# Optimization experiments

Measured on AMD Instinct MI355X. Metric: run time of the kernel, lower is better.

## Reference

```python
import jax, jax.numpy as jnp
import numpy as np

B, CIN, COUT, H, W = 64, 64, 64, 32, 32
K, STRIDE, PAD = 3, 1, 1
HOUT = (H + 2 * PAD - K) // STRIDE + 1
WOUT = (W + 2 * PAD - K) // STRIDE + 1


def setup_inputs() -> dict:
    key = jax.random.key(0)
    k1, k2, k3 = jax.random.split(key, 3)
    x = jax.random.normal(k1, (B, CIN, H, W), dtype=jnp.float32)
    # weight: per-location filters (leading singleton batch dim of the torch
    # param is dropped; it only served broadcasting)
    weight = jax.random.normal(k2, (CIN, COUT, HOUT, WOUT, K, K), dtype=jnp.float32)
    bias = jax.random.normal(k3, (COUT, HOUT, WOUT), dtype=jnp.float32)
    return {"x": x, "weight": weight, "bias": bias}


def _extract_patches(x, k, stride, pad, hout, wout):
    # x: [B, C, H, W] -> patches [B, C, k*k, hout, wout]
    xp = jnp.pad(x, ((0, 0), (0, 0), (pad, pad), (pad, pad)))
    slabs = [
        xp[:, :, i : i + (hout - 1) * stride + 1 : stride,
               j : j + (wout - 1) * stride + 1 : stride]
        for i in range(k) for j in range(k)
    ]
    return jnp.stack(slabs, axis=2)


def reference(x, weight, bias):
    cin, cout, hout, wout, k, _ = weight.shape
    patches = _extract_patches(x, k, STRIDE, PAD, hout, wout)  # [B, Cin, k*k, Ho, Wo]
    w = weight.reshape(cin, cout, hout, wout, k * k)
    # fused per-location dot product: avoids the [B,Cin,Cout,Ho,Wo,k,k] intermediate
    y = jnp.einsum('bikhw,iohwk->bohw', patches, w) + bias[None]
    return y
```

## Files before the change

### kernel.cpp

```cpp
#include <hip/hip_runtime.h>
#include <hip/hip_bf16.h>


#define B_    64
#define HW_   32
#define HP_   34
#define NLOC  1024
#define W_OST 9216u
#define W_IST 589824u
#define XT_BYTES  ((size_t)64*HP_*HP_*64*2)
#define AF_BYTES  ((size_t)NLOC*18*4*64*16)
#define WS_NEED   (XT_BYTES + AF_BYTES)

typedef __attribute__((ext_vector_type(8))) short short8;
typedef __attribute__((ext_vector_type(8))) unsigned short ushort8;
typedef __attribute__((ext_vector_type(4))) float floatx4;

static __device__ __forceinline__ unsigned short f2bf(float f) {
  __hip_bfloat16 h = __float2bfloat16(f);
  return __builtin_bit_cast(unsigned short, h);
}

__global__ __launch_bounds__(256) void xpose_pad(const float* __restrict__ x,
                                                 unsigned short* __restrict__ xt) {
  int bid = blockIdx.x;
  int i = bid / HP_, hh = bid % HP_;
  __shared__ float tile[B_ * 33];
  int t = threadIdx.x;
  bool interior = (hh >= 1 && hh <= HW_);
  if (interior) {
    int h = hh - 1, w = t & 31, bs = t >> 5;
    #pragma unroll
    for (int r = 0; r < 8; ++r) {
      int b = r * 8 + bs;
      tile[b * 33 + w] = x[(((size_t)b * 64 + i) * HW_ + h) * HW_ + w];
    }
  }
  __syncthreads();
  int b = t & 63, wsb = t >> 6;
  size_t base = (size_t)(i * HP_ + hh) * HP_ * B_;
  #pragma unroll
  for (int s = 0; s < 9; ++s) {
    int ww = s * 4 + wsb;
    if (ww < HP_) {
      float v = 0.f;
      if (interior && ww >= 1 && ww <= HW_) v = tile[b * 33 + (ww - 1)];
      xt[base + (size_t)ww * B_ + b] = f2bf(v);
    }
  }
}

__global__ __launch_bounds__(256) void im2col_frag(
    const unsigned short* __restrict__ xt,
    unsigned short* __restrict__ af) {
  __shared__ unsigned short scr[4][512];
  const int bid  = blockIdx.x;
  const int loc  = ((bid & 7) << 7) | (bid >> 3);
  const int hblk = loc >> 5, wblk = loc & 31;
  const int tid  = threadIdx.x;
  const int lane = tid & 63;
  const int wv   = tid >> 6;

  #pragma unroll 1
  for (int c = 0; c < 18; ++c) {
    int i, kh, kw;
    if (c < 16) {
      i = (c << 2) + wv;
      int kk = lane >> 3;
      kh = kk / 3; kw = kk - kh * 3;
    } else {
      i = (c - 16) * 32 + wv * 8 + (lane >> 3);
      kh = 2; kw = 2;
    }
    const ushort8* src = (const ushort8*)(xt +
        (((unsigned)i * HP_ + (unsigned)(hblk + kh)) * HP_ + (unsigned)(wblk + kw)) * 64u
        + ((unsigned)(lane & 7) << 3));
    ushort8 v = *src;
    *(ushort8*)&scr[wv][lane << 3] = v;
    __asm__ volatile("s_waitcnt lgkmcnt(0)" ::: "memory");
    ushort8 p;
    #pragma unroll
    for (int jr = 0; jr < 8; ++jr) p[jr] = scr[wv][jr * 64 + lane];
    __asm__ volatile("s_waitcnt lgkmcnt(0)" ::: "memory");
    size_t slot = ((size_t)(loc * 18 + c) * 4 + (size_t)(lane >> 4)) * 64
                + (size_t)((lane & 15) + (wv << 4));
    *(ushort8*)(af + (slot << 3)) = p;
  }
}

__global__ __launch_bounds__(512, 2) void lc2d_fused(
    const unsigned short* __restrict__ af,
    const float* __restrict__ wsrc,
    const float* __restrict__ bias,
    float* __restrict__ out) {
  __shared__ unsigned short Bf[2][4 * 4 * 64 * 8];
  __shared__ unsigned short Bs[4 * 2 * 4 * 64 * 8];

  const int bid  = blockIdx.x;
  const int loc0 = bid << 2;
  const int tid  = threadIdx.x;
  const int lane = tid & 63;
  const int wv8  = tid >> 6;
  const int ll   = wv8 >> 1;
  const int nh   = wv8 & 1;
  const int loc  = loc0 + ll;
  const int col  = lane & 15;
  const int quad = lane >> 4;
  const int o_0  = nh * 32 + col;

  floatx4 acc[4][2];
  {
    float b0 = bias[(unsigned)o_0 * 1024u + (unsigned)loc];
    float b1 = bias[(unsigned)(o_0 + 16) * 1024u + (unsigned)loc];
    #pragma unroll
    for (int mt = 0; mt < 4; ++mt) {
      acc[mt][0] = (floatx4){b0, b0, b0, b0};
      acc[mt][1] = (floatx4){b1, b1, b1, b1};
    }
  }

  floatx4 wreg[5];
  const bool lastok = (tid < 256);
  const size_t wrow = (size_t)loc0 * 9;

  auto issueW = [&](int c) {
    const int i0 = c << 2;
    #pragma unroll
    for (int r = 0; r < 5; ++r) {
      if (r < 4 || lastok) {
        int idx = r * 512 + tid;
        int g = idx / 9, p = idx - g * 9;
        int i = i0 + (g >> 6), o = g & 63;
        wreg[r] = *(const floatx4*)(wsrc + (size_t)i * W_IST + (size_t)o * W_OST
                                    + wrow + (size_t)(p * 4));
      }
    }
  };
  auto scatterW = [&](int c, int buf) {
    const int i0 = c << 2;
    #pragma unroll
    for (int r = 0; r < 5; ++r) {
      if (r < 4 || lastok) {
        int idx = r * 512 + tid;
        int g = idx / 9, p = idx - g * 9;
        int iq = g >> 6, o = g & 63;
        int ot = o >> 4, oc = o & 15;
        int flane = iq * 16 + oc;
        #pragma unroll
        for (int e = 0; e < 4; ++e) {
          int fi = p * 4 + e;
          int lle = fi / 9, kk = fi - lle * 9;
          unsigned short v = f2bf(wreg[r][e]);
          if (kk < 8) {
            Bf[buf][((lle * 4 + ot) * 64 + flane) * 8 + kk] = v;
          } else {
            int i = i0 + iq;
            int sc = i >> 5, k2 = i & 31;
            Bs[((lle * 8 + sc * 4 + ot) * 64 + (k2 >> 3) * 16 + oc) * 8 + (k2 & 7)] = v;
          }
        }
      }
    }
  };

  const size_t abase = (size_t)loc * (18 * 4 * 64 * 8) + ((size_t)lane << 3);
  auto ldA = [&](int c, int tl) {
    return *(const ushort8*)(af + abase + ((size_t)(c * 4 + tl) << 9));
  };

  ushort8 pa0 = ldA(0, 0), pa1 = ldA(0, 1), pa2 = ldA(0, 2), pa3 = ldA(0, 3);

  issueW(0);
  scatterW(0, 0);
  __syncthreads();

  int buf = 0;
  #pragma unroll 1
  for (int c = 0; c < 16; ++c) {
    if (c < 15) issueW(c + 1);
    ushort8 a0 = pa0, a1 = pa1, a2 = pa2, a3 = pa3;
    pa0 = ldA(c + 1, 0); pa1 = ldA(c + 1, 1);
    pa2 = ldA(c + 1, 2); pa3 = ldA(c + 1, 3);
    ushort8 b0 = *(const ushort8*)&Bf[buf][((ll * 4 + nh * 2 + 0) * 64 + lane) * 8];
    ushort8 b1 = *(const ushort8*)&Bf[buf][((ll * 4 + nh * 2 + 1) * 64 + lane) * 8];
    acc[0][0] = __builtin_amdgcn_mfma_f32_16x16x32_bf16(
        __builtin_bit_cast(short8, a0), __builtin_bit_cast(short8, b0), acc[0][0], 0, 0, 0);
    acc[1][0] = __builtin_amdgcn_mfma_f32_16x16x32_bf16(
        __builtin_bit_cast(short8, a1), __builtin_bit_cast(short8, b0), acc[1][0], 0, 0, 0);
    acc[2][0] = __builtin_amdgcn_mfma_f32_16x16x32_bf16(
        __builtin_bit_cast(short8, a2), __builtin_bit_cast(short8, b0), acc[2][0], 0, 0, 0);
    acc[3][0] = __builtin_amdgcn_mfma_f32_16x16x32_bf16(
        __builtin_bit_cast(short8, a3), __builtin_bit_cast(short8, b0), acc[3][0], 0, 0, 0);
    acc[0][1] = __builtin_amdgcn_mfma_f32_16x16x32_bf16(
        __builtin_bit_cast(short8, a0), __builtin_bit_cast(short8, b1), acc[0][1], 0, 0, 0);
    acc[1][1] = __builtin_amdgcn_mfma_f32_16x16x32_bf16(
        __builtin_bit_cast(short8, a1), __builtin_bit_cast(short8, b1), acc[1][1], 0, 0, 0);
    acc[2][1] = __builtin_amdgcn_mfma_f32_16x16x32_bf16(
        __builtin_bit_cast(short8, a2), __builtin_bit_cast(short8, b1), acc[2][1], 0, 0, 0);
    acc[3][1] = __builtin_amdgcn_mfma_f32_16x16x32_bf16(
        __builtin_bit_cast(short8, a3), __builtin_bit_cast(short8, b1), acc[3][1], 0, 0, 0);
    if (c < 15) scatterW(c + 1, buf ^ 1);
    __syncthreads();
    buf ^= 1;
  }

  #pragma unroll
  for (int sc = 0; sc < 2; ++sc) {
    ushort8 a0 = pa0, a1 = pa1, a2 = pa2, a3 = pa3;
    if (sc == 0) { pa0 = ldA(17, 0); pa1 = ldA(17, 1); pa2 = ldA(17, 2); pa3 = ldA(17, 3); }
    ushort8 b0 = *(const ushort8*)&Bs[((ll * 8 + sc * 4 + nh * 2 + 0) * 64 + lane) * 8];
    ushort8 b1 = *(const ushort8*)&Bs[((ll * 8 + sc * 4 + nh * 2 + 1) * 64 + lane) * 8];
    acc[0][0] = __builtin_amdgcn_mfma_f32_16x16x32_bf16(
        __builtin_bit_cast(short8, a0), __builtin_bit_cast(short8, b0), acc[0][0], 0, 0, 0);
    acc[1][0] = __builtin_amdgcn_mfma_f32_16x16x32_bf16(
        __builtin_bit_cast(short8, a1), __builtin_bit_cast(short8, b0), acc[1][0], 0, 0, 0);
    acc[2][0] = __builtin_amdgcn_mfma_f32_16x16x32_bf16(
        __builtin_bit_cast(short8, a2), __builtin_bit_cast(short8, b0), acc[2][0], 0, 0, 0);
    acc[3][0] = __builtin_amdgcn_mfma_f32_16x16x32_bf16(
        __builtin_bit_cast(short8, a3), __builtin_bit_cast(short8, b0), acc[3][0], 0, 0, 0);
    acc[0][1] = __builtin_amdgcn_mfma_f32_16x16x32_bf16(
        __builtin_bit_cast(short8, a0), __builtin_bit_cast(short8, b1), acc[0][1], 0, 0, 0);
    acc[1][1] = __builtin_amdgcn_mfma_f32_16x16x32_bf16(
        __builtin_bit_cast(short8, a1), __builtin_bit_cast(short8, b1), acc[1][1], 0, 0, 0);
    acc[2][1] = __builtin_amdgcn_mfma_f32_16x16x32_bf16(
        __builtin_bit_cast(short8, a2), __builtin_bit_cast(short8, b1), acc[2][1], 0, 0, 0);
    acc[3][1] = __builtin_amdgcn_mfma_f32_16x16x32_bf16(
        __builtin_bit_cast(short8, a3), __builtin_bit_cast(short8, b1), acc[3][1], 0, 0, 0);
  }

  #pragma unroll
  for (int mt = 0; mt < 4; ++mt) {
    int b = mt * 16 + quad * 4;
    #pragma unroll
    for (int r = 0; r < 4; ++r) {
      out[((unsigned)(b + r) * 64u + (unsigned)o_0) * 1024u + (unsigned)loc] = acc[mt][0][r];
      out[((unsigned)(b + r) * 64u + (unsigned)(o_0 + 16)) * 1024u + (unsigned)loc] = acc[mt][1][r];
    }
  }
}

__global__ __launch_bounds__(256, 4) void lc2d_fallback(
    const float* __restrict__ x, const float* __restrict__ weight,
    const float* __restrict__ bias, float* __restrict__ out) {
  int t0 = blockIdx.x;
  int loc = ((t0 & 7) << 7) | (t0 >> 3);
  int h = loc >> 5, w = loc & 31;
  int tid = threadIdx.x;
  int b = tid & 63;
  int o0 = (tid >> 6) * 16;
  __shared__ float As[72 * 64];
  float acc[16];
  #pragma unroll
  for (int j = 0; j < 16; ++j) acc[j] = bias[(size_t)(o0 + j) * NLOC + loc];
  for (int ic = 0; ic < 8; ++ic) {
    __syncthreads();
    #pragma unroll
    for (int s = 0; s < 18; ++s) {
      int f = s * 256 + tid;
      int k = f >> 6, lb = f & 63;
      int kk = k >> 3, isub = k & 7;
      int i = ic * 8 + isub;
      int kh = kk / 3, kw = kk - kh * 3;
      int hh = h + kh - 1, ww = w + kw - 1;
      float v = (hh >= 0 && hh < HW_ && ww >= 0 && ww < HW_)
                  ? x[(((size_t)lb * 64 + i) * HW_ + hh) * HW_ + ww] : 0.f;
      As[k * 64 + lb] = v;
    }
    __syncthreads();
    #pragma unroll 1
    for (int isub = 0; isub < 8; ++isub) {
      const float* wp = weight + (size_t)(ic * 8 + isub) * W_IST
                               + (size_t)o0 * W_OST + loc * 9;
      #pragma unroll
      for (int kk = 0; kk < 9; ++kk) {
        float a = As[(kk * 8 + isub) * 64 + b];
        #pragma unroll
        for (int j = 0; j < 16; ++j)
          acc[j] = fmaf(a, wp[(size_t)j * W_OST + kk], acc[j]);
      }
    }
  }
  size_t ob = ((size_t)b * 64 + o0) * NLOC + loc;
  #pragma unroll
  for (int j = 0; j < 16; ++j) out[ob + (size_t)j * NLOC] = acc[j];
}

extern "C" void kernel_launch(void* const* d_in, const int* in_sizes, int n_in,
                              void* d_out, int out_size, void* d_ws, size_t ws_size,
                              hipStream_t stream) {
  const float* x  = (const float*)d_in[0];
  const float* wt = (const float*)d_in[1];
  const float* bs = (const float*)d_in[2];
  float* out = (float*)d_out;

  if (ws_size >= WS_NEED) {
    unsigned short* xtb = (unsigned short*)d_ws;
    unsigned short* af  = (unsigned short*)((char*)d_ws + XT_BYTES);
    xpose_pad<<<64 * HP_, 256, 0, stream>>>(x, xtb);
    im2col_frag<<<NLOC, 256, 0, stream>>>(xtb, af);
    lc2d_fused<<<NLOC / 4, 512, 0, stream>>>(af, wt, bs, out);
  } else {
    lc2d_fallback<<<NLOC, 256, 0, stream>>>(x, wt, bs, out);
  }
}
```

Before: 286.9 us.

## Fuse im2col fragment build into the locally-connected MFMA kernel

```diff
diff --git a/kernel.cpp b/kernel.cpp
--- a/kernel.cpp
+++ b/kernel.cpp
@@ -9,8 +9,7 @@
 #define W_OST 9216u
 #define W_IST 589824u
 #define XT_BYTES  ((size_t)64*HP_*HP_*64*2)
-#define AF_BYTES  ((size_t)NLOC*18*4*64*16)
-#define WS_NEED   (XT_BYTES + AF_BYTES)
+#define WS_NEED   (XT_BYTES)
 
 typedef __attribute__((ext_vector_type(8))) short short8;
 typedef __attribute__((ext_vector_type(8))) unsigned short ushort8;
@@ -50,51 +49,15 @@
   }
 }
 
-__global__ __launch_bounds__(256) void im2col_frag(
+__global__ __launch_bounds__(512, 2) void lc2d_fused(
     const unsigned short* __restrict__ xt,
-    unsigned short* __restrict__ af) {
-  __shared__ unsigned short scr[4][512];
-  const int bid  = blockIdx.x;
-  const int loc  = ((bid & 7) << 7) | (bid >> 3);
-  const int hblk = loc >> 5, wblk = loc & 31;
-  const int tid  = threadIdx.x;
-  const int lane = tid & 63;
-  const int wv   = tid >> 6;
-
-  #pragma unroll 1
-  for (int c = 0; c < 18; ++c) {
-    int i, kh, kw;
-    if (c < 16) {
-      i = (c << 2) + wv;
-      int kk = lane >> 3;
-      kh = kk / 3; kw = kk - kh * 3;
-    } else {
-      i = (c - 16) * 32 + wv * 8 + (lane >> 3);
-      kh = 2; kw = 2;
-    }
-    const ushort8* src = (const ushort8*)(xt +
-        (((unsigned)i * HP_ + (unsigned)(hblk + kh)) * HP_ + (unsigned)(wblk + kw)) * 64u
-        + ((unsigned)(lane & 7) << 3));
-    ushort8 v = *src;
-    *(ushort8*)&scr[wv][lane << 3] = v;
-    __asm__ volatile("s_waitcnt lgkmcnt(0)" ::: "memory");
-    ushort8 p;
-    #pragma unroll
-    for (int jr = 0; jr < 8; ++jr) p[jr] = scr[wv][jr * 64 + lane];
-    __asm__ volatile("s_waitcnt lgkmcnt(0)" ::: "memory");
-    size_t slot = ((size_t)(loc * 18 + c) * 4 + (size_t)(lane >> 4)) * 64
-                + (size_t)((lane & 15) + (wv << 4));
-    *(ushort8*)(af + (slot << 3)) = p;
-  }
-}
-
-__global__ __launch_bounds__(512, 2) void lc2d_fused(
-    const unsigned short* __restrict__ af,
     const float* __restrict__ wsrc,
     const float* __restrict__ bias,
     float* __restrict__ out) {
-  __shared__ unsigned short Bf[2][4 * 4 * 64 * 8];
-  __shared__ unsigned short Bs[4 * 2 * 4 * 64 * 8];
+  __shared__ __align__(16) unsigned short Af[2][4 * 4 * 64 * 8];
+  __shared__ __align__(16) unsigned short Bf[2][4 * 4 * 64 * 8];
+  __shared__ __align__(16) unsigned short Bs[4 * 2 * 4 * 64 * 8];
+  __shared__ __align__(16) unsigned short scr[8][512];
 
   const int bid  = blockIdx.x;
   const int loc0 = bid << 2;
@@ -104,6 +67,7 @@
   const int ll   = wv8 >> 1;
   const int nh   = wv8 & 1;
   const int loc  = loc0 + ll;
+  const int hblk = loc >> 5, wblk = loc & 31;
   const int col  = lane & 15;
   const int quad = lane >> 4;
   const int o_0  = nh * 32 + col;
@@ -119,11 +83,11 @@
     }
   }
 
-  floatx4 wreg[5];
+  floatx4 wa[5], wb[5];
   const bool lastok = (tid < 256);
   const size_t wrow = (size_t)loc0 * 9;
 
-  auto issueW = [&](int c) {
+  auto issueW = [&](int c, floatx4 (&wreg)[5]) {
     const int i0 = c << 2;
     #pragma unroll
     for (int r = 0; r < 5; ++r) {
@@ -136,7 +100,7 @@
       }
     }
   };
-  auto scatterW = [&](int c, int buf) {
+  auto scatterW = [&](int c, floatx4 (&wreg)[5], unsigned short* bfp) {
     const int i0 = c << 2;
     #pragma unroll
     for (int r = 0; r < 5; ++r) {
@@ -152,7 +116,7 @@
           int lle = fi / 9, kk = fi - lle * 9;
           unsigned short v = f2bf(wreg[r][e]);
           if (kk < 8) {
-            Bf[buf][((lle * 4 + ot) * 64 + flane) * 8 + kk] = v;
+            bfp[((lle * 4 + ot) * 64 + flane) * 8 + kk] = v;
           } else {
             int i = i0 + iq;
             int sc = i >> 5, k2 = i & 31;
@@ -163,26 +127,40 @@
     }
   };
 
-  const size_t abase = (size_t)loc * (18 * 4 * 64 * 8) + ((size_t)lane << 3);
-  auto ldA = [&](int c, int tl) {
-    return *(const ushort8*)(af + abase + ((size_t)(c * 4 + tl) << 9));
-  };
-
-  ushort8 pa0 = ldA(0, 0), pa1 = ldA(0, 1), pa2 = ldA(0, 2), pa3 = ldA(0, 3);
-
-  issueW(0);
-  scatterW(0, 0);
-  __syncthreads();
-
-  int buf = 0;
-  #pragma unroll 1
-  for (int c = 0; c < 16; ++c) {
-    if (c < 15) issueW(c + 1);
-    ushort8 a0 = pa0, a1 = pa1, a2 = pa2, a3 = pa3;
-    pa0 = ldA(c + 1, 0); pa1 = ldA(c + 1, 1);
-    pa2 = ldA(c + 1, 2); pa3 = ldA(c + 1, 3);
-    ushort8 b0 = *(const ushort8*)&Bf[buf][((ll * 4 + nh * 2 + 0) * 64 + lane) * 8];
-    ushort8 b1 = *(const ushort8*)&Bf[buf][((ll * 4 + nh * 2 + 1) * 64 + lane) * 8];
+  auto xtLoad = [&](int t, int s) -> ushort8 {
+    int q = (nh << 1) + s;
+    int i, kh, kw;
+    if (t < 16) {
+      i = (t << 2) + q;
+      int kk = lane >> 3;
+      kh = kk / 3; kw = kk - kh * 3;
+    } else {
+      i = ((t - 16) << 5) + (q << 3) + (lane >> 3);
+      kh = 2; kw = 2;
+    }
+    return *(const ushort8*)(xt +
+        (((unsigned)i * HP_ + (unsigned)(hblk + kh)) * HP_ + (unsigned)(wblk + kw)) * 64u
+        + ((unsigned)(lane & 7) << 3));
+  };
+  auto xposeStore = [&](ushort8 v, int s, unsigned short* afp) {
+    const int q = (nh << 1) + s;
+    *(ushort8*)&scr[wv8][lane << 3] = v;
+    __asm__ volatile("s_waitcnt lgkmcnt(0)" ::: "memory");
+    ushort8 p;
+    #pragma unroll
+    for (int jr = 0; jr < 8; ++jr) p[jr] = scr[wv8][jr * 64 + lane];
+    __asm__ volatile("s_waitcnt lgkmcnt(0)" ::: "memory");
+    *(ushort8*)(afp + (size_t)((((ll << 2) + (lane >> 4)) << 6)
+                               + (q << 4) + (lane & 15)) * 8) = p;
+  };
+
+  auto doMFMA = [&](const unsigned short* afp, const unsigned short* bbase, int boff) {
+    ushort8 a0 = *(const ushort8*)(afp + (size_t)(((ll << 2) + 0) * 64 + lane) * 8);
+    ushort8 a1 = *(const ushort8*)(afp + (size_t)(((ll << 2) + 1) * 64 + lane) * 8);
+    ushort8 a2 = *(const ushort8*)(afp + (size_t)(((ll << 2) + 2) * 64 + lane) * 8);
+    ushort8 a3 = *(const ushort8*)(afp + (size_t)(((ll << 2) + 3) * 64 + lane) * 8);
+    ushort8 b0 = *(const ushort8*)(bbase + (size_t)((boff + 0) * 64 + lane) * 8);
+    ushort8 b1 = *(const ushort8*)(bbase + (size_t)((boff + 1) * 64 + lane) * 8);
     acc[0][0] = __builtin_amdgcn_mfma_f32_16x16x32_bf16(
         __builtin_bit_cast(short8, a0), __builtin_bit_cast(short8, b0), acc[0][0], 0, 0, 0);
     acc[1][0] = __builtin_amdgcn_mfma_f32_16x16x32_bf16(
@@ -199,33 +177,46 @@
         __builtin_bit_cast(short8, a2), __builtin_bit_cast(short8, b1), acc[2][1], 0, 0, 0);
     acc[3][1] = __builtin_amdgcn_mfma_f32_16x16x32_bf16(
         __builtin_bit_cast(short8, a3), __builtin_bit_cast(short8, b1), acc[3][1], 0, 0, 0);
-    if (c < 15) scatterW(c + 1, buf ^ 1);
+  };
+
+  issueW(0, wa);
+  {
+    ushort8 pv0 = xtLoad(0, 0);
+    ushort8 pv1 = xtLoad(0, 1);
+    xposeStore(pv0, 0, &Af[0][0]);
+    xposeStore(pv1, 1, &Af[0][0]);
+  }
+  scatterW(0, wa, &Bf[0][0]);
+  issueW(1, wb);
+  __syncthreads();
+
+#define STEP(C, WI, WS) do {                                                  \
+    const int c_ = (C);                                                       \
+    ushort8 xv0 = xtLoad(c_ + 1, 0);                                          \
+    ushort8 xv1 = xtLoad(c_ + 1, 1);                                          \
+    if (c_ + 2 <= 15) issueW(c_ + 2, WI);                                     \
+    doMFMA(&Af[c_ & 1][0], &Bf[c_ & 1][0], (ll << 2) + (nh << 1));            \
+    xposeStore(xv0, 0, &Af[(c_ & 1) ^ 1][0]);                                 \
+    xposeStore(xv1, 1, &Af[(c_ & 1) ^ 1][0]);                                 \
+    if (c_ + 1 <= 15) scatterW(c_ + 1, WS, &Bf[(c_ & 1) ^ 1][0]);             \
+    __syncthreads();                                                          \
+  } while (0)
+
+  #pragma unroll 1
+  for (int cc = 0; cc < 16; cc += 2) {
+    STEP(cc,     wa, wb);
+    STEP(cc + 1, wb, wa);
+  }
+#undef STEP
+
+  {
+    ushort8 xv0 = xtLoad(17, 0);
+    ushort8 xv1 = xtLoad(17, 1);
+    doMFMA(&Af[0][0], &Bs[0], (ll << 3) + 0 + (nh << 1));
+    xposeStore(xv0, 0, &Af[1][0]);
+    xposeStore(xv1, 1, &Af[1][0]);
     __syncthreads();
-    buf ^= 1;
-  }
-
-  #pragma unroll
-  for (int sc = 0; sc < 2; ++sc) {
-    ushort8 a0 = pa0, a1 = pa1, a2 = pa2, a3 = pa3;
-    if (sc == 0) { pa0 = ldA(17, 0); pa1 = ldA(17, 1); pa2 = ldA(17, 2); pa3 = ldA(17, 3); }
-    ushort8 b0 = *(const ushort8*)&Bs[((ll * 8 + sc * 4 + nh * 2 + 0) * 64 + lane) * 8];
-    ushort8 b1 = *(const ushort8*)&Bs[((ll * 8 + sc * 4 + nh * 2 + 1) * 64 + lane) * 8];
-    acc[0][0] = __builtin_amdgcn_mfma_f32_16x16x32_bf16(
-        __builtin_bit_cast(short8, a0), __builtin_bit_cast(short8, b0), acc[0][0], 0, 0, 0);
-    acc[1][0] = __builtin_amdgcn_mfma_f32_16x16x32_bf16(
-        __builtin_bit_cast(short8, a1), __builtin_bit_cast(short8, b0), acc[1][0], 0, 0, 0);
-    acc[2][0] = __builtin_amdgcn_mfma_f32_16x16x32_bf16(
-        __builtin_bit_cast(short8, a2), __builtin_bit_cast(short8, b0), acc[2][0], 0, 0, 0);
-    acc[3][0] = __builtin_amdgcn_mfma_f32_16x16x32_bf16(
-        __builtin_bit_cast(short8, a3), __builtin_bit_cast(short8, b0), acc[3][0], 0, 0, 0);
-    acc[0][1] = __builtin_amdgcn_mfma_f32_16x16x32_bf16(
-        __builtin_bit_cast(short8, a0), __builtin_bit_cast(short8, b1), acc[0][1], 0, 0, 0);
-    acc[1][1] = __builtin_amdgcn_mfma_f32_16x16x32_bf16(
-        __builtin_bit_cast(short8, a1), __builtin_bit_cast(short8, b1), acc[1][1], 0, 0, 0);
-    acc[2][1] = __builtin_amdgcn_mfma_f32_16x16x32_bf16(
-        __builtin_bit_cast(short8, a2), __builtin_bit_cast(short8, b1), acc[2][1], 0, 0, 0);
-    acc[3][1] = __builtin_amdgcn_mfma_f32_16x16x32_bf16(
-        __builtin_bit_cast(short8, a3), __builtin_bit_cast(short8, b1), acc[3][1], 0, 0, 0);
+    doMFMA(&Af[1][0], &Bs[0], (ll << 3) + 4 + (nh << 1));
   }
 
   #pragma unroll
@@ -295,10 +286,8 @@
 
   if (ws_size >= WS_NEED) {
     unsigned short* xtb = (unsigned short*)d_ws;
-    unsigned short* af  = (unsigned short*)((char*)d_ws + XT_BYTES);
     xpose_pad<<<64 * HP_, 256, 0, stream>>>(x, xtb);
-    im2col_frag<<<NLOC, 256, 0, stream>>>(xtb, af);
-    lc2d_fused<<<NLOC / 4, 512, 0, stream>>>(af, wt, bs, out);
+    lc2d_fused<<<NLOC / 4, 512, 0, stream>>>(xtb, wt, bs, out);
   } else {
     lc2d_fallback<<<NLOC, 256, 0, stream>>>(x, wt, bs, out);
   }
```

After: 263.6 us. 8.1% less time.
